# Performance work log

Hardware: AMD Instinct MI355X
Metric: run time of the kernel (lower is better)

## Reference

```python
import jax, jax.numpy as jnp
import numpy as np

B, C, H, W = 16, 256, 56, 56
G, K, R = 16, 3, 2
CR = C // R          # reduced channels = 128
KKG = K * K * G      # span output channels = 144
EPS = 1e-5


def setup_inputs() -> dict:
    key = jax.random.key(0)
    ks = jax.random.split(key, 5)
    return {
        "x": jax.random.normal(ks[0], (B, C, H, W), jnp.float32),
        "w_reduce": jax.random.normal(ks[1], (CR, C), jnp.float32) * 0.05,
        "b_reduce": jax.random.normal(ks[2], (CR,), jnp.float32) * 0.05,
        "gamma": jnp.ones((CR,), jnp.float32),
        "beta": jnp.zeros((CR,), jnp.float32),
        "w_span": jax.random.normal(ks[3], (KKG, CR), jnp.float32) * 0.05,
        "b_span": jax.random.normal(ks[4], (KKG,), jnp.float32) * 0.05,
    }


def _conv1x1(x, w, bias):
    # 1x1 conv == channel contraction
    return jnp.einsum('bchw,oc->bohw', x, w) + bias[None, :, None, None]


def _involution(x, w_reduce, b_reduce, gamma, beta, w_span, b_span):
    b, c, h, w = x.shape
    # kernel-generation branch: reduce -> BN (batch stats) -> ReLU -> span
    t = _conv1x1(x, w_reduce, b_reduce)
    mu = t.mean(axis=(0, 2, 3), keepdims=True)
    var = t.var(axis=(0, 2, 3), keepdims=True)  # biased, as torch BN training
    t = (t - mu) * jax.lax.rsqrt(var + EPS)
    t = t * gamma[None, :, None, None] + beta[None, :, None, None]
    t = jax.nn.relu(t)
    kern = _conv1x1(t, w_span, b_span)  # [b, k*k*g, h, w]
    # 'b (k j g) h w -> b g (k j) h w'
    kern = kern.reshape(b, K, K, G, h, w).transpose(0, 3, 1, 2, 4, 5)
    kern = kern.reshape(b, G, K * K, h, w)
    # unfold x into [b, g, d, k*k, h, w] via shifted padded slices (no dense im2col buffer write pattern beyond necessity)
    p = K // 2
    xp = jnp.pad(x, ((0, 0), (0, 0), (p, p), (p, p)))
    patches = jnp.stack(
        [xp[:, :, i:i + h, j:j + w] for i in range(K) for j in range(K)],
        axis=2)  # [b, c, k*k, h, w]
    patches = patches.reshape(b, G, c // G, K * K, h, w)
    out = jnp.einsum('bgdxhw,bgxhw->bgdhw', patches, kern)  # weighted window sum
    return out.reshape(b, c, h, w)


def reference(x, w_reduce, b_reduce, gamma, beta, w_span, b_span):
    return _involution(x, w_reduce, b_reduce, gamma, beta, w_span, b_span)
```

## Files before the change

kernel.cpp:

```cpp
#include <hip/hip_runtime.h>

#define B_   16
#define C_   256
#define HW_  3136
#define W_   56
#define CR_  128
#define KKG_ 144
#define G_   16
#define NPOS (B_*HW_)
#define EPS_ 1e-5f
#define NBLK 784

typedef float f32x4 __attribute__((ext_vector_type(4)));
typedef short s16x8 __attribute__((ext_vector_type(8)));
typedef short s16x4 __attribute__((ext_vector_type(4)));

#define T2_OFF_B    0
#define KERN_OFF_B  12845056
#define GP_OFF_B    27295744
#define STAT_OFF_B  28098560
#define WBFR_OFF_B  28099584
#define WBFS_OFF_B  28165120

__device__ inline unsigned short f2bf(float f) {
    unsigned u = __float_as_uint(f);
    u += 0x7fff + ((u >> 16) & 1);
    return (unsigned short)(u >> 16);
}
__device__ inline float bf2f(unsigned short h) {
    return __uint_as_float(((unsigned)h) << 16);
}

__global__ __launch_bounds__(256) void prep_cast(
    const float* __restrict__ w_reduce, const float* __restrict__ w_span,
    unsigned short* __restrict__ wbfr, unsigned short* __restrict__ wbfs)
{
    int idx = blockIdx.x * 256 + threadIdx.x;
    if (idx < 32768) {
        wbfr[idx] = f2bf(w_reduce[idx]);
    } else {
        int k = idx - 32768;
        if (k < 18432) wbfs[k] = f2bf(w_span[k]);
    }
}

__global__ __launch_bounds__(256) void reduce_mfma(
    const float* __restrict__ x, const unsigned short* __restrict__ wbfr,
    unsigned short* __restrict__ t2, float* __restrict__ gp)
{
    __shared__ __align__(16) short as_[128 * 40];
    __shared__ __align__(16) short bs_[64 * 40];
    __shared__ float redp[128][2], redq[128][2];

    const int tid = threadIdx.x;
    const int lane = tid & 63, wv = tid >> 6;
    const int q = lane >> 4, i = lane & 15;
    const int mrow = (wv >> 1) * 64, nrow = (wv & 1) * 32;
    const int blk = blockIdx.x;
    const int b = blk / 49;
    const int p0 = (blk % 49) * 64;

    const float* xb = x + (size_t)b * C_ * HW_ + p0;

    const int o_a = tid >> 1, half = tid & 1;
    const int cp = tid >> 4, rq = tid & 15;

    f32x4 acc[4][2] = {};

    for (int c0 = 0; c0 < C_; c0 += 32) {
        {
            const unsigned short* src = wbfr + o_a * C_ + c0 + half * 16;
            s16x8 w0 = *(const s16x8*)src;
            s16x8 w1 = *(const s16x8*)(src + 8);
            *(s16x8*)&as_[o_a * 40 + half * 16] = w0;
            *(s16x8*)&as_[o_a * 40 + half * 16 + 8] = w1;
        }
        {
            const float* s0 = xb + (size_t)(c0 + 2 * cp) * HW_ + rq * 4;
            float4 va = *(const float4*)s0;
            float4 vb = *(const float4*)(s0 + HW_);
            float a4[4] = {va.x, va.y, va.z, va.w};
            float b4[4] = {vb.x, vb.y, vb.z, vb.w};
            #pragma unroll
            for (int j = 0; j < 4; j++) {
                unsigned pk = (unsigned)f2bf(a4[j]) | ((unsigned)f2bf(b4[j]) << 16);
                *(unsigned*)&bs_[(rq * 4 + j) * 40 + 2 * cp] = pk;
            }
        }
        __syncthreads();
        s16x8 af[4], bfr[2];
        #pragma unroll
        for (int mt = 0; mt < 4; mt++)
            af[mt] = *(const s16x8*)&as_[(mrow + mt * 16 + i) * 40 + q * 8];
        #pragma unroll
        for (int nt = 0; nt < 2; nt++)
            bfr[nt] = *(const s16x8*)&bs_[(nrow + nt * 16 + i) * 40 + q * 8];
        #pragma unroll
        for (int mt = 0; mt < 4; mt++)
            #pragma unroll
            for (int nt = 0; nt < 2; nt++)
                acc[mt][nt] = __builtin_amdgcn_mfma_f32_16x16x32_bf16(
                    af[mt], bfr[nt], acc[mt][nt], 0, 0, 0);
        __syncthreads();
    }

    #pragma unroll
    for (int mt = 0; mt < 4; mt++) {
        #pragma unroll
        for (int nt = 0; nt < 2; nt++) {
            #pragma unroll
            for (int reg = 0; reg < 4; reg++) {
                int o = mrow + mt * 16 + q * 4 + reg;
                int p = p0 + nrow + nt * 16 + i;
                t2[((size_t)o * B_ + b) * HW_ + p] = f2bf(acc[mt][nt][reg]);
            }
        }
        #pragma unroll
        for (int reg = 0; reg < 4; reg++) {
            float v0 = acc[mt][0][reg], v1 = acc[mt][1][reg];
            float s = v0 + v1;
            float ss = v0 * v0 + v1 * v1;
            #pragma unroll
            for (int m = 1; m < 16; m <<= 1) {
                s  += __shfl_xor(s, m);
                ss += __shfl_xor(ss, m);
            }
            if (i == 0) {
                int o = mrow + mt * 16 + q * 4 + reg;
                redp[o][wv & 1] = s;
                redq[o][wv & 1] = ss;
            }
        }
    }
    __syncthreads();
    if (tid < 128)
        gp[(size_t)blk * 256 + tid] = redp[tid][0] + redp[tid][1];
    else
        gp[(size_t)blk * 256 + tid] = redq[tid - 128][0] + redq[tid - 128][1];
}

__global__ __launch_bounds__(256) void bn_finalize(
    const float* __restrict__ gp, const float* __restrict__ gamma,
    const float* __restrict__ beta, float* __restrict__ stats)
{
    const int o = blockIdx.x;
    const int tid = threadIdx.x;
    float s = 0.f, ss = 0.f;
    for (int blk = tid; blk < NBLK; blk += 256) {
        s  += gp[(size_t)blk * 256 + o];
        ss += gp[(size_t)blk * 256 + 128 + o];
    }
    #pragma unroll
    for (int m = 1; m < 64; m <<= 1) {
        s  += __shfl_xor(s, m);
        ss += __shfl_xor(ss, m);
    }
    __shared__ float rs[4], rss[4];
    if ((tid & 63) == 0) { rs[tid >> 6] = s; rss[tid >> 6] = ss; }
    __syncthreads();
    if (tid == 0) {
        s  = rs[0] + rs[1] + rs[2] + rs[3];
        ss = rss[0] + rss[1] + rss[2] + rss[3];
        float inv_n = 1.0f / (float)NPOS;
        float mu = s * inv_n;
        float var = ss * inv_n - mu * mu;
        float sc = gamma[o] * rsqrtf(var + EPS_);
        stats[o] = sc;
        stats[128 + o] = beta[o] - mu * sc;
    }
}

__global__ __launch_bounds__(256) void span_mfma(
    const unsigned short* __restrict__ t2, const unsigned short* __restrict__ wbfs,
    const float* __restrict__ b_span, const float* __restrict__ stats,
    unsigned short* __restrict__ kern)
{
    __shared__ __align__(16) short as_[144 * 40];
    __shared__ __align__(16) short bs_[64 * 40];
    __shared__ float scs[128], shs[128], bsp[144];

    const int tid = threadIdx.x;
    const int lane = tid & 63, wv = tid >> 6;
    const int q = lane >> 4, i = lane & 15;
    const int blk = blockIdx.x;
    const int b = blk / 49;
    const int p0 = (blk % 49) * 64;

    if (tid < 128) { scs[tid] = stats[tid]; shs[tid] = stats[128 + tid]; }
    if (tid < 144) bsp[tid] = b_span[tid];
    __syncthreads();

    const int op = tid >> 4, seg = tid & 15;

    f32x4 acc[9] = {};

    for (int c0 = 0; c0 < CR_; c0 += 32) {
        #pragma unroll
        for (int P = 0; P < 3; P++) {
            int idx = P * 256 + tid;
            if (idx < 576) {
                int row = idx >> 2, k8 = idx & 3;
                *(s16x8*)&as_[row * 40 + k8 * 8] =
                    *(const s16x8*)&wbfs[row * CR_ + c0 + k8 * 8];
            }
        }
        {
            int cA = c0 + 2 * op;
            const unsigned short* tA = t2 + ((size_t)cA * B_ + b) * HW_ + p0 + seg * 4;
            s16x4 vA = *(const s16x4*)tA;
            s16x4 vB = *(const s16x4*)(tA + (size_t)B_ * HW_);
            float sA = scs[cA], hA = shs[cA];
            float sB = scs[cA + 1], hB = shs[cA + 1];
            #pragma unroll
            for (int j = 0; j < 4; j++) {
                float fa = fmaxf(fmaf(bf2f((unsigned short)vA[j]), sA, hA), 0.0f);
                float fb = fmaxf(fmaf(bf2f((unsigned short)vB[j]), sB, hB), 0.0f);
                unsigned pk = (unsigned)f2bf(fa) | ((unsigned)f2bf(fb) << 16);
                *(unsigned*)&bs_[(seg * 4 + j) * 40 + 2 * op] = pk;
            }
        }
        __syncthreads();
        s16x8 bfrag = *(const s16x8*)&bs_[(wv * 16 + i) * 40 + q * 8];
        #pragma unroll
        for (int mt = 0; mt < 9; mt++) {
            s16x8 af = *(const s16x8*)&as_[(mt * 16 + i) * 40 + q * 8];
            acc[mt] = __builtin_amdgcn_mfma_f32_16x16x32_bf16(af, bfrag, acc[mt], 0, 0, 0);
        }
        __syncthreads();
    }

    const int p = p0 + wv * 16 + i;
    #pragma unroll
    for (int mt = 0; mt < 9; mt++) {
        #pragma unroll
        for (int reg = 0; reg < 4; reg++) {
            int o2 = mt * 16 + q * 4 + reg;
            kern[((size_t)b * KKG_ + o2) * HW_ + p] = f2bf(acc[mt][reg] + bsp[o2]);
        }
    }
}

__global__ __launch_bounds__(256) void involution_apply(
    const float* __restrict__ x, const unsigned short* __restrict__ kern,
    float* __restrict__ out)
{
    int gtid = blockIdx.x * 256 + threadIdx.x;
    int pix = gtid % HW_;
    int bg  = gtid / HW_;
    int g = bg & 15;
    int b = bg >> 4;
    int h = pix / W_;
    int w = pix % W_;

    const unsigned short* kb = kern + (size_t)b * KKG_ * HW_ + pix;
    float kv[9];
    #pragma unroll
    for (int kk = 0; kk < 9; kk++)
        kv[kk] = bf2f(kb[(size_t)(kk * G_ + g) * HW_]);

    float acc[16];
    #pragma unroll
    for (int d = 0; d < 16; d++) acc[d] = 0.0f;

    const float* xb = x + (size_t)(b * C_ + g * 16) * HW_;
    #pragma unroll
    for (int di = 0; di < 3; di++) {
        int hh = h + di - 1;
        if (hh < 0 || hh >= W_) continue;
        #pragma unroll
        for (int dj = 0; dj < 3; dj++) {
            int ww = w + dj - 1;
            if (ww < 0 || ww >= W_) continue;
            float kval = kv[di * 3 + dj];
            int off = hh * W_ + ww;
            #pragma unroll
            for (int d = 0; d < 16; d++)
                acc[d] = fmaf(xb[(size_t)d * HW_ + off], kval, acc[d]);
        }
    }
    float* ob = out + (size_t)(b * C_ + g * 16) * HW_ + pix;
    #pragma unroll
    for (int d = 0; d < 16; d++) ob[(size_t)d * HW_] = acc[d];
}

extern "C" void kernel_launch(void* const* d_in, const int* in_sizes, int n_in,
                              void* d_out, int out_size, void* d_ws, size_t ws_size,
                              hipStream_t stream) {
    const float* x        = (const float*)d_in[0];
    const float* w_reduce = (const float*)d_in[1];
    const float* gamma    = (const float*)d_in[3];
    const float* beta     = (const float*)d_in[4];
    const float* w_span   = (const float*)d_in[5];
    const float* b_span   = (const float*)d_in[6];
    float* out = (float*)d_out;

    char* wsb = (char*)d_ws;
    unsigned short* t2   = (unsigned short*)(wsb + T2_OFF_B);
    unsigned short* kern = (unsigned short*)(wsb + KERN_OFF_B);
    float*          gp    = (float*)(wsb + GP_OFF_B);
    float*          stats = (float*)(wsb + STAT_OFF_B);
    unsigned short* wbfr = (unsigned short*)(wsb + WBFR_OFF_B);
    unsigned short* wbfs = (unsigned short*)(wsb + WBFS_OFF_B);

    prep_cast<<<200, 256, 0, stream>>>(w_reduce, w_span, wbfr, wbfs);
    reduce_mfma<<<NBLK, 256, 0, stream>>>(x, wbfr, t2, gp);
    bn_finalize<<<128, 256, 0, stream>>>(gp, gamma, beta, stats);
    span_mfma<<<NBLK, 256, 0, stream>>>(t2, wbfs, b_span, stats, kern);
    involution_apply<<<(B_ * G_ * HW_) / 256, 256, 0, stream>>>(x, kern, out);
}
```

Before: 161.5 us.

## Drop LDS staging in both GEMMs, load fragments directly with register prefetch

```diff
diff --git a/kernel.cpp b/kernel.cpp
--- a/kernel.cpp
+++ b/kernel.cpp
@@ -1,4 +1,5 @@
 #include <hip/hip_runtime.h>
+#include <hip/hip_bf16.h>
 
 #define B_   16
 #define C_   256
@@ -9,18 +10,18 @@
 #define G_   16
 #define NPOS (B_*HW_)
 #define EPS_ 1e-5f
-#define NBLK 784
+#define NBLK1 1568
+#define NBLK3 784
 
 typedef float f32x4 __attribute__((ext_vector_type(4)));
 typedef short s16x8 __attribute__((ext_vector_type(8)));
-typedef short s16x4 __attribute__((ext_vector_type(4)));
 
 #define T2_OFF_B    0
 #define KERN_OFF_B  12845056
 #define GP_OFF_B    27295744
-#define STAT_OFF_B  28098560
-#define WBFR_OFF_B  28099584
-#define WBFS_OFF_B  28165120
+#define STAT_OFF_B  28901376
+#define WBFR_OFF_B  28902400
+#define WBFS_OFF_B  28967936
 
 __device__ inline unsigned short f2bf(float f) {
     unsigned u = __float_as_uint(f);
@@ -29,6 +30,12 @@
 }
 __device__ inline float bf2f(unsigned short h) {
     return __uint_as_float(((unsigned)h) << 16);
+}
+__device__ inline unsigned pkcvt(float a, float b) {
+    float2 f2; f2.x = a; f2.y = b;
+    __hip_bfloat162 h = __float22bfloat162_rn(f2);
+    union { __hip_bfloat162 h2; unsigned u; } cv; cv.h2 = h;
+    return cv.u;
 }
 
 __global__ __launch_bounds__(256) void prep_cast(
@@ -44,99 +51,88 @@
     }
 }
 
-__global__ __launch_bounds__(256) void reduce_mfma(
+__global__ __launch_bounds__(256, 5) void reduce_mfma(
     const float* __restrict__ x, const unsigned short* __restrict__ wbfr,
     unsigned short* __restrict__ t2, float* __restrict__ gp)
 {
-    __shared__ __align__(16) short as_[128 * 40];
-    __shared__ __align__(16) short bs_[64 * 40];
     __shared__ float redp[128][2], redq[128][2];
 
     const int tid = threadIdx.x;
     const int lane = tid & 63, wv = tid >> 6;
     const int q = lane >> 4, i = lane & 15;
-    const int mrow = (wv >> 1) * 64, nrow = (wv & 1) * 32;
+    const int q8 = q * 8;
+    const int ow = (wv & 1) * 64;
+    const int psel = wv >> 1;
     const int blk = blockIdx.x;
-    const int b = blk / 49;
-    const int p0 = (blk % 49) * 64;
-
-    const float* xb = x + (size_t)b * C_ * HW_ + p0;
-
-    const int o_a = tid >> 1, half = tid & 1;
-    const int cp = tid >> 4, rq = tid & 15;
-
-    f32x4 acc[4][2] = {};
-
-    for (int c0 = 0; c0 < C_; c0 += 32) {
-        {
-            const unsigned short* src = wbfr + o_a * C_ + c0 + half * 16;
-            s16x8 w0 = *(const s16x8*)src;
-            s16x8 w1 = *(const s16x8*)(src + 8);
-            *(s16x8*)&as_[o_a * 40 + half * 16] = w0;
-            *(s16x8*)&as_[o_a * 40 + half * 16 + 8] = w1;
-        }
-        {
-            const float* s0 = xb + (size_t)(c0 + 2 * cp) * HW_ + rq * 4;
-            float4 va = *(const float4*)s0;
-            float4 vb = *(const float4*)(s0 + HW_);
-            float a4[4] = {va.x, va.y, va.z, va.w};
-            float b4[4] = {vb.x, vb.y, vb.z, vb.w};
-            #pragma unroll
-            for (int j = 0; j < 4; j++) {
-                unsigned pk = (unsigned)f2bf(a4[j]) | ((unsigned)f2bf(b4[j]) << 16);
-                *(unsigned*)&bs_[(rq * 4 + j) * 40 + 2 * cp] = pk;
-            }
-        }
-        __syncthreads();
-        s16x8 af[4], bfr[2];
+    const int b = blk / 98;
+    const int p0 = (blk % 98) * 32;
+    const int pw = p0 + psel * 16;
+
+    const float* xcol = x + (size_t)b * C_ * HW_ + pw + i;
+    const unsigned short* wrow = wbfr + (size_t)(ow + i) * C_ + q8;
+
+    f32x4 acc[4] = {};
+
+    float Bc[8], Bn[8];
+    s16x8 Ac[4], An[4];
+    #pragma unroll
+    for (int k = 0; k < 8; k++) Bc[k] = xcol[(size_t)(q8 + k) * HW_];
+    #pragma unroll
+    for (int mt = 0; mt < 4; mt++)
+        Ac[mt] = *(const s16x8*)(wrow + (size_t)mt * 16 * C_);
+
+    #pragma unroll
+    for (int ch = 0; ch < 8; ch++) {
+        const int c0 = ch * 32;
+        if (ch < 7) {
+            #pragma unroll
+            for (int k = 0; k < 8; k++)
+                Bn[k] = xcol[(size_t)(c0 + 32 + q8 + k) * HW_];
+            #pragma unroll
+            for (int mt = 0; mt < 4; mt++)
+                An[mt] = *(const s16x8*)(wrow + (size_t)mt * 16 * C_ + c0 + 32);
+        }
+        union { s16x8 v; unsigned u[4]; } Bv;
+        #pragma unroll
+        for (int k2 = 0; k2 < 4; k2++) Bv.u[k2] = pkcvt(Bc[2*k2], Bc[2*k2+1]);
         #pragma unroll
         for (int mt = 0; mt < 4; mt++)
-            af[mt] = *(const s16x8*)&as_[(mrow + mt * 16 + i) * 40 + q * 8];
-        #pragma unroll
-        for (int nt = 0; nt < 2; nt++)
-            bfr[nt] = *(const s16x8*)&bs_[(nrow + nt * 16 + i) * 40 + q * 8];
-        #pragma unroll
-        for (int mt = 0; mt < 4; mt++)
-            #pragma unroll
-            for (int nt = 0; nt < 2; nt++)
-                acc[mt][nt] = __builtin_amdgcn_mfma_f32_16x16x32_bf16(
-                    af[mt], bfr[nt], acc[mt][nt], 0, 0, 0);
-        __syncthreads();
-    }
-
+            acc[mt] = __builtin_amdgcn_mfma_f32_16x16x32_bf16(
+                Ac[mt], Bv.v, acc[mt], 0, 0, 0);
+        #pragma unroll
+        for (int k = 0; k < 8; k++) Bc[k] = Bn[k];
+        #pragma unroll
+        for (int mt = 0; mt < 4; mt++) Ac[mt] = An[mt];
+    }
+
+    const int p = pw + i;
     #pragma unroll
     for (int mt = 0; mt < 4; mt++) {
-        #pragma unroll
-        for (int nt = 0; nt < 2; nt++) {
-            #pragma unroll
-            for (int reg = 0; reg < 4; reg++) {
-                int o = mrow + mt * 16 + q * 4 + reg;
-                int p = p0 + nrow + nt * 16 + i;
-                t2[((size_t)o * B_ + b) * HW_ + p] = f2bf(acc[mt][nt][reg]);
-            }
-        }
+        uint2 pr;
+        pr.x = pkcvt(acc[mt][0], acc[mt][1]);
+        pr.y = pkcvt(acc[mt][2], acc[mt][3]);
+        *(uint2*)(t2 + ((size_t)b * HW_ + p) * CR_ + ow + mt * 16 + q * 4) = pr;
         #pragma unroll
         for (int reg = 0; reg < 4; reg++) {
-            float v0 = acc[mt][0][reg], v1 = acc[mt][1][reg];
-            float s = v0 + v1;
-            float ss = v0 * v0 + v1 * v1;
+            float v = acc[mt][reg];
+            float s = v, ss = v * v;
             #pragma unroll
             for (int m = 1; m < 16; m <<= 1) {
                 s  += __shfl_xor(s, m);
                 ss += __shfl_xor(ss, m);
             }
             if (i == 0) {
-                int o = mrow + mt * 16 + q * 4 + reg;
-                redp[o][wv & 1] = s;
-                redq[o][wv & 1] = ss;
+                int o = ow + mt * 16 + q * 4 + reg;
+                redp[o][psel] = s;
+                redq[o][psel] = ss;
             }
         }
     }
     __syncthreads();
     if (tid < 128)
-        gp[(size_t)blk * 256 + tid] = redp[tid][0] + redp[tid][1];
+        gp[(size_t)tid * NBLK1 + blk] = redp[tid][0] + redp[tid][1];
     else
-        gp[(size_t)blk * 256 + tid] = redq[tid - 128][0] + redq[tid - 128][1];
+        gp[(size_t)tid * NBLK1 + blk] = redq[tid - 128][0] + redq[tid - 128][1];
 }
 
 __global__ __launch_bounds__(256) void bn_finalize(
@@ -146,9 +142,9 @@
     const int o = blockIdx.x;
     const int tid = threadIdx.x;
     float s = 0.f, ss = 0.f;
-    for (int blk = tid; blk < NBLK; blk += 256) {
-        s  += gp[(size_t)blk * 256 + o];
-        ss += gp[(size_t)blk * 256 + 128 + o];
+    for (int idx = tid; idx < NBLK1; idx += 256) {
+        s  += gp[(size_t)o * NBLK1 + idx];
+        ss += gp[(size_t)(128 + o) * NBLK1 + idx];
     }
     #pragma unroll
     for (int m = 1; m < 64; m <<= 1) {
@@ -170,72 +166,76 @@
     }
 }
 
-__global__ __launch_bounds__(256) void span_mfma(
+__global__ __launch_bounds__(256, 3) void span_mfma(
     const unsigned short* __restrict__ t2, const unsigned short* __restrict__ wbfs,
     const float* __restrict__ b_span, const float* __restrict__ stats,
     unsigned short* __restrict__ kern)
 {
-    __shared__ __align__(16) short as_[144 * 40];
-    __shared__ __align__(16) short bs_[64 * 40];
     __shared__ float scs[128], shs[128], bsp[144];
 
     const int tid = threadIdx.x;
     const int lane = tid & 63, wv = tid >> 6;
     const int q = lane >> 4, i = lane & 15;
+    const int q8 = q * 8;
     const int blk = blockIdx.x;
     const int b = blk / 49;
-    const int p0 = (blk % 49) * 64;
-
-    if (tid < 128) { scs[tid] = stats[tid]; shs[tid] = stats[128 + tid]; }
+    const int pw = (blk % 49) * 64 + wv * 16;
+
+    const unsigned short* trow = t2 + ((size_t)b * HW_ + pw + i) * CR_ + q8;
+    const unsigned short* wrow = wbfs + (size_t)i * CR_ + q8;
+
+    s16x8 Bc, Bn;
+    s16x8 Ac[9], An[9];
+    Bc = *(const s16x8*)trow;
+    #pragma unroll
+    for (int mt = 0; mt < 9; mt++)
+        Ac[mt] = *(const s16x8*)(wrow + (size_t)mt * 16 * CR_);
+
+    if (tid < 128) {
+        scs[tid] = stats[tid];
+        shs[tid] = stats[128 + tid];
+    }
     if (tid < 144) bsp[tid] = b_span[tid];
     __syncthreads();
 
-    const int op = tid >> 4, seg = tid & 15;
-
     f32x4 acc[9] = {};
 
-    for (int c0 = 0; c0 < CR_; c0 += 32) {
-        #pragma unroll
-        for (int P = 0; P < 3; P++) {
-            int idx = P * 256 + tid;
-            if (idx < 576) {
-                int row = idx >> 2, k8 = idx & 3;
-                *(s16x8*)&as_[row * 40 + k8 * 8] =
-                    *(const s16x8*)&wbfs[row * CR_ + c0 + k8 * 8];
-            }
-        }
-        {
-            int cA = c0 + 2 * op;
-            const unsigned short* tA = t2 + ((size_t)cA * B_ + b) * HW_ + p0 + seg * 4;
-            s16x4 vA = *(const s16x4*)tA;
-            s16x4 vB = *(const s16x4*)(tA + (size_t)B_ * HW_);
-            float sA = scs[cA], hA = shs[cA];
-            float sB = scs[cA + 1], hB = shs[cA + 1];
-            #pragma unroll
-            for (int j = 0; j < 4; j++) {
-                float fa = fmaxf(fmaf(bf2f((unsigned short)vA[j]), sA, hA), 0.0f);
-                float fb = fmaxf(fmaf(bf2f((unsigned short)vB[j]), sB, hB), 0.0f);
-                unsigned pk = (unsigned)f2bf(fa) | ((unsigned)f2bf(fb) << 16);
-                *(unsigned*)&bs_[(seg * 4 + j) * 40 + 2 * op] = pk;
-            }
-        }
-        __syncthreads();
-        s16x8 bfrag = *(const s16x8*)&bs_[(wv * 16 + i) * 40 + q * 8];
-        #pragma unroll
-        for (int mt = 0; mt < 9; mt++) {
-            s16x8 af = *(const s16x8*)&as_[(mt * 16 + i) * 40 + q * 8];
-            acc[mt] = __builtin_amdgcn_mfma_f32_16x16x32_bf16(af, bfrag, acc[mt], 0, 0, 0);
-        }
-        __syncthreads();
-    }
-
-    const int p = p0 + wv * 16 + i;
+    #pragma unroll
+    for (int ch = 0; ch < 4; ch++) {
+        const int c0 = ch * 32;
+        if (ch < 3) {
+            Bn = *(const s16x8*)(trow + c0 + 32);
+            #pragma unroll
+            for (int mt = 0; mt < 9; mt++)
+                An[mt] = *(const s16x8*)(wrow + (size_t)mt * 16 * CR_ + c0 + 32);
+        }
+        const int cb = c0 + q8;
+        float f[8];
+        #pragma unroll
+        for (int k = 0; k < 8; k++)
+            f[k] = fmaxf(fmaf(bf2f((unsigned short)Bc[k]),
+                              scs[cb + k], shs[cb + k]), 0.0f);
+        union { s16x8 v; unsigned u[4]; } Bv;
+        #pragma unroll
+        for (int k2 = 0; k2 < 4; k2++) Bv.u[k2] = pkcvt(f[2*k2], f[2*k2+1]);
+
+        #pragma unroll
+        for (int mt = 0; mt < 9; mt++)
+            acc[mt] = __builtin_amdgcn_mfma_f32_16x16x32_bf16(
+                Ac[mt], Bv.v, acc[mt], 0, 0, 0);
+        Bc = Bn;
+        #pragma unroll
+        for (int mt = 0; mt < 9; mt++) Ac[mt] = An[mt];
+    }
+
+    const int p = pw + i;
     #pragma unroll
     for (int mt = 0; mt < 9; mt++) {
         #pragma unroll
         for (int reg = 0; reg < 4; reg++) {
             int o2 = mt * 16 + q * 4 + reg;
-            kern[((size_t)b * KKG_ + o2) * HW_ + p] = f2bf(acc[mt][reg] + bsp[o2]);
+            int row = (o2 & 15) * 9 + (o2 >> 4);
+            kern[((size_t)b * KKG_ + row) * HW_ + p] = f2bf(acc[mt][reg] + bsp[o2]);
         }
     }
 }
@@ -252,11 +252,11 @@
     int h = pix / W_;
     int w = pix % W_;
 
-    const unsigned short* kb = kern + (size_t)b * KKG_ * HW_ + pix;
+    const unsigned short* kb = kern + ((size_t)(b * G_ + g) * 9) * HW_ + pix;
     float kv[9];
     #pragma unroll
     for (int kk = 0; kk < 9; kk++)
-        kv[kk] = bf2f(kb[(size_t)(kk * G_ + g) * HW_]);
+        kv[kk] = bf2f(kb[(size_t)kk * HW_]);
 
     float acc[16];
     #pragma unroll
@@ -303,8 +303,8 @@
     unsigned short* wbfs = (unsigned short*)(wsb + WBFS_OFF_B);
 
     prep_cast<<<200, 256, 0, stream>>>(w_reduce, w_span, wbfr, wbfs);
-    reduce_mfma<<<NBLK, 256, 0, stream>>>(x, wbfr, t2, gp);
+    reduce_mfma<<<NBLK1, 256, 0, stream>>>(x, wbfr, t2, gp);
     bn_finalize<<<128, 256, 0, stream>>>(gp, gamma, beta, stats);
-    span_mfma<<<NBLK, 256, 0, stream>>>(t2, wbfs, b_span, stats, kern);
+    span_mfma<<<NBLK3, 256, 0, stream>>>(t2, wbfs, b_span, stats, kern);
     involution_apply<<<(B_ * G_ * HW_) / 256, 256, 0, stream>>>(x, kern, out);
 }
```

Result: slower. 192.3 us (+19.0%).
